# Performance work log

Hardware: AMD Instinct MI355X
Metric: run time of the kernel (lower is better)

Reference implementation:

```python
import jax, jax.numpy as jnp
import numpy as np

B, C, W, H, HEADS = 32, 512, 32, 32, 8
D = C // HEADS
N = W * H
LN_EPS = 1e-5


def setup_inputs() -> dict:
    key = jax.random.key(0)
    ks = jax.random.split(key, 11)
    s = 1.0 / np.sqrt(C)
    return {
        "x": jax.random.normal(ks[0], (B, C, W, H), jnp.float32),
        "Wq": jax.random.normal(ks[1], (C, C), jnp.float32) * s,
        "bq": jax.random.normal(ks[2], (C,), jnp.float32) * 0.01,
        "Wk": jax.random.normal(ks[3], (C, C), jnp.float32) * s,
        "bk": jax.random.normal(ks[4], (C,), jnp.float32) * 0.01,
        "Wv": jax.random.normal(ks[5], (C, C), jnp.float32) * s,
        "bv": jax.random.normal(ks[6], (C,), jnp.float32) * 0.01,
        "rel_h": jax.random.normal(ks[7], (1, HEADS, D, 1, H), jnp.float32),
        "rel_w": jax.random.normal(ks[8], (1, HEADS, D, W, 1), jnp.float32),
        "ln_w": jnp.ones((C, W, H), jnp.float32),
        "ln_b": jnp.zeros((C, W, H), jnp.float32),
    }


def reference(x, Wq, bq, Wk, bk, Wv, bv, rel_h, rel_w, ln_w, ln_b):
    b, c, w, h = x.shape
    nh, d, n = HEADS, c // HEADS, w * h

    def proj(Wm, bm):
        # 1x1 conv == per-pixel linear: out[b,o,w,h] = sum_c Wm[o,c] x[b,c,w,h] + bm[o]
        y = jnp.einsum('bcwh,oc->bowh', x, Wm) + bm[None, :, None, None]
        return y.reshape(b, nh, d, n)

    q = proj(Wq, bq)  # [B,h,d,N]
    k = proj(Wk, bk)
    v = proj(Wv, bv)

    # content-content: q^T k -> [B,h,N,N]
    cc = jnp.einsum('bhdn,bhdm->bhnm', q, k)
    # content-position: (rel_h + rel_w) flattened to [h,d,N], permuted, matmul with q
    pos = (rel_h + rel_w).reshape(nh, d, n)  # [h,d,N]
    cp = jnp.einsum('hdn,bhdm->bhnm', pos, q)

    attn = jax.nn.softmax(cc + cp, axis=-1)  # [B,h,N,N]
    # out = v @ attn^T  -> [B,h,d,N]
    out = jnp.einsum('bhdn,bhmn->bhdm', v, attn)
    out = out.reshape(b, c, w, h)

    # LayerNorm over [C,W,H] with elementwise affine, then residual
    mu = jnp.mean(out, axis=(1, 2, 3), keepdims=True)
    var = jnp.var(out, axis=(1, 2, 3), keepdims=True)
    out = (out - mu) * jax.lax.rsqrt(var + LN_EPS) * ln_w[None] + ln_b[None]
    return out + x
```

## Files before the change

kernel.cpp:

```cpp
#include <hip/hip_runtime.h>
#include <stdint.h>

typedef _Float16 f16x8 __attribute__((ext_vector_type(8)));
typedef _Float16 f16x4 __attribute__((ext_vector_type(4)));
typedef __fp16   fp16x2 __attribute__((ext_vector_type(2)));
typedef float f32x4  __attribute__((ext_vector_type(4)));

__device__ __forceinline__ _Float16 f2h(float f){ return (_Float16)f; }

__device__ __forceinline__ void gl16(const void* g, void* l){
  __builtin_amdgcn_global_load_lds((const __attribute__((address_space(1))) void*)g,
                                   (__attribute__((address_space(3))) void*)l, 16, 0, 0);
}

#define NB   32
#define NC   512
#define NH   8
#define ND   64
#define NN   1024

#define LOG2E 1.44269504f

__global__ __launch_bounds__(256) void wt_conv(const float* __restrict__ Wq,
                                               const float* __restrict__ Wk,
                                               const float* __restrict__ Wv,
                                               _Float16* __restrict__ Wt){
  int idx = blockIdx.x * 256 + threadIdx.x;
  int sel = idx >> 18;
  const float* W = (sel == 0) ? Wq : (sel == 1) ? Wk : Wv;
  Wt[idx] = f2h(W[idx & 262143]);
}

__global__ __launch_bounds__(256) void transpose_x(const float* __restrict__ x,
                                                   _Float16* __restrict__ xT){
  __shared__ float tile[32][33];
  int n0 = blockIdx.x * 32, c0 = blockIdx.y * 32, b = blockIdx.z;
  int t = threadIdx.x;
  int tn = t & 31, tc = t >> 5;
#pragma unroll
  for (int k = 0; k < 4; k++)
    tile[tc + 8*k][tn] = x[(b*NC + c0 + tc + 8*k)*NN + n0 + tn];
  __syncthreads();
#pragma unroll
  for (int k = 0; k < 4; k++)
    xT[(b*NN + n0 + tc + 8*k)*NC + c0 + tn] = f2h(tile[tn][tc + 8*k]);
}

__global__ __launch_bounds__(256) void pos_conv(const float* __restrict__ rel_h,
                                                const float* __restrict__ rel_w,
                                                _Float16* __restrict__ pos_t){
  int idx = blockIdx.x * 256 + threadIdx.x;
  int d = idx & 63, n = (idx >> 6) & 1023, h = idx >> 16;
  int ww = n >> 5, hh = n & 31;
  float v = rel_h[(h*ND + d)*32 + hh] + rel_w[(h*ND + d)*32 + ww];
  pos_t[idx] = f2h(v);
}

#define TSTR 136

__global__ __launch_bounds__(256) void proj_gemm(const _Float16* __restrict__ Wt,
                                                 const _Float16* __restrict__ xT,
                                                 const float* __restrict__ bq,
                                                 const float* __restrict__ bk,
                                                 const float* __restrict__ bv,
                                                 _Float16* __restrict__ q_ws,
                                                 _Float16* __restrict__ k_ws,
                                                 _Float16* __restrict__ v_ws){
  __shared__ _Float16 smem[17408];
  _Float16* As = smem;
  _Float16* Bs = smem + 8192;

  int mt = blockIdx.x;
  int nt = blockIdx.y;
  int b  = blockIdx.z;
  int t = threadIdx.x, lane = t & 63, w = t >> 6;
  int wm = w >> 1, wn = w & 1;
  int lr = lane & 15, lg = lane >> 4;

  f32x4 acc[4][4];
#pragma unroll
  for (int i = 0; i < 4; i++)
#pragma unroll
    for (int j = 0; j < 4; j++) acc[i][j] = (f32x4)0.f;

  const _Float16* Arow = Wt + mt * 128 * NC;
  const _Float16* Brow = xT + (b * NN + nt * 128) * NC;

  int s_r8 = lane >> 3;
  int s_g  = lane & 7;

  for (int k0 = 0; k0 < NC; k0 += 64){
    __syncthreads();
#pragma unroll
    for (int i = 0; i < 4; i++){
      int r0  = w*32 + i*8;
      int row = r0 + s_r8;
      int gx  = (s_g ^ (row & 7)) << 3;
      gl16(Arow + row*NC + k0 + gx, As + r0*64);
      gl16(Brow + row*NC + k0 + gx, Bs + r0*64);
    }
    __syncthreads();
#pragma unroll
    for (int ks = 0; ks < 2; ks++){
      int xg = (((ks << 2) | lg) ^ (lr & 7)) << 3;
      f16x8 af[4], bfr[4];
#pragma unroll
      for (int mi = 0; mi < 4; mi++)
        af[mi] = *(f16x8*)(As + (wm*64 + mi*16 + lr)*64 + xg);
#pragma unroll
      for (int nj = 0; nj < 4; nj++)
        bfr[nj] = *(f16x8*)(Bs + (wn*64 + nj*16 + lr)*64 + xg);
      __builtin_amdgcn_s_setprio(1);
#pragma unroll
      for (int mi = 0; mi < 4; mi++)
#pragma unroll
        for (int nj = 0; nj < 4; nj++)
          acc[mi][nj] = __builtin_amdgcn_mfma_f32_16x16x32_f16(af[mi], bfr[nj], acc[mi][nj], 0, 0, 0);
      __builtin_amdgcn_s_setprio(0);
    }
  }
  __syncthreads();

  if (mt < 8){
    _Float16* Ts = smem;
#pragma unroll
    for (int mi = 0; mi < 4; mi++){
      int o0 = wm*64 + mi*16 + 4*lg;
      int og = mt*128 + o0;
      int sel = og >> 9, oo = og & 511;
      const float* bias = (sel == 0) ? bq : bk;
      float sc = (sel == 0) ? LOG2E : 1.f;
      float b0 = bias[oo], b1 = bias[oo+1], b2 = bias[oo+2], b3 = bias[oo+3];
#pragma unroll
      for (int nj = 0; nj < 4; nj++){
        int pix = wn*64 + nj*16 + lr;
        f16x4 pk;
        pk[0] = f2h((acc[mi][nj][0] + b0) * sc);
        pk[1] = f2h((acc[mi][nj][1] + b1) * sc);
        pk[2] = f2h((acc[mi][nj][2] + b2) * sc);
        pk[3] = f2h((acc[mi][nj][3] + b3) * sc);
        *(f16x4*)(Ts + pix*TSTR + o0) = pk;
      }
    }
    __syncthreads();
#pragma unroll
    for (int i = 0; i < 8; i++){
      int lin = t + 256 * i;
      int c_o = lin & 15, pix = lin >> 4;
      f16x8 v = *(f16x8*)(Ts + pix*TSTR + c_o*8);
      int og = mt*128 + c_o*8;
      int sel = og >> 9, oo = og & 511;
      int head = oo >> 6, d = oo & 63;
      _Float16* dst = (sel == 0) ? q_ws : k_ws;
      *(f16x8*)(dst + (((b*NH + head)*NN) + nt*128 + pix)*ND + d) = v;
    }
  } else {
    _Float16* Ts2 = smem;
#pragma unroll
    for (int mi = 0; mi < 4; mi++){
      int o0 = wm*64 + mi*16 + 4*lg;
      int vb = (mt - 8)*128 + o0;
      float b0 = bv[vb], b1 = bv[vb+1], b2 = bv[vb+2], b3 = bv[vb+3];
#pragma unroll
      for (int nj = 0; nj < 4; nj++){
        int pix = wn*64 + nj*16 + lr;
        Ts2[(o0+0)*TSTR + pix] = f2h(acc[mi][nj][0] + b0);
        Ts2[(o0+1)*TSTR + pix] = f2h(acc[mi][nj][1] + b1);
        Ts2[(o0+2)*TSTR + pix] = f2h(acc[mi][nj][2] + b2);
        Ts2[(o0+3)*TSTR + pix] = f2h(acc[mi][nj][3] + b3);
      }
    }
    __syncthreads();
#pragma unroll
    for (int i = 0; i < 8; i++){
      int lin = t + 256 * i;
      int pix8 = lin & 15, o_loc = lin >> 4;
      f16x8 v = *(f16x8*)(Ts2 + o_loc*TSTR + pix8*8);
      int vb = (mt - 8)*128 + o_loc;
      int head = vb >> 6, d = vb & 63;
      *(f16x8*)(v_ws + ((b*NH + head)*ND + d)*NN + nt*128 + pix8*8) = v;
    }
  }
}

#define KSTR 136
#define PSTR 72
#define OSTR 65
#define OFF_VT 8704
#define OFF_P  12800

__global__ __launch_bounds__(256, 3) void attn_kernel(const _Float16* __restrict__ q_ws,
                                                      const _Float16* __restrict__ k_ws,
                                                      const _Float16* __restrict__ v_ws,
                                                      const _Float16* __restrict__ pos_t,
                                                      _Float16* __restrict__ o16,
                                                      float* __restrict__ red){
  __shared__ _Float16 smem[22016];
  __shared__ float lnred[8];
  _Float16* Kc = smem;
  _Float16* Vt = smem + OFF_VT;
  _Float16* Pl = smem + OFF_P;

  int bid = blockIdx.x;
  int sid = (bid & 7) * 256 + (bid >> 3);
  int qt = sid & 7, h = (sid >> 3) & 7, b = sid >> 6;

  int t = threadIdx.x, lane = t & 63, w = t >> 6;
  int lr = lane & 15, lg = lane >> 4;

  const _Float16* qbh = q_ws + (b*NH + h) * NN * ND;
  const _Float16* kbh = k_ws + (b*NH + h) * NN * ND;
  const _Float16* vbh = v_ws + (b*NH + h) * ND * NN;
  const _Float16* pph = pos_t + h * NN * ND;

  f16x8 qreg[2][4];
#pragma unroll
  for (int qi = 0; qi < 2; qi++){
    int row = qt*128 + w*32 + qi*16 + lr;
#pragma unroll
    for (int ks = 0; ks < 4; ks++){
      const _Float16* src = (ks < 2) ? (qbh + row*ND + ks*32 + lg*8)
                                     : (pph + row*ND + (ks-2)*32 + lg*8);
      qreg[qi][ks] = *(const f16x8*)src;
    }
  }

  f16x8 ones;
#pragma unroll
  for (int e = 0; e < 8; e++) ones[e] = (_Float16)1.f;

  float m_r[2];
  f32x4 oacc[2][4];
  f32x4 lacc[2];
#pragma unroll
  for (int qi = 0; qi < 2; qi++){ m_r[qi] = -1e30f; lacc[qi] = (f32x4)0.f; }
#pragma unroll
  for (int qi = 0; qi < 2; qi++)
#pragma unroll
    for (int dj = 0; dj < 4; dj++) oacc[qi][dj] = (f32x4)0.f;

  for (int n0 = 0; n0 < NN; n0 += 64){
    __syncthreads();
#pragma unroll
    for (int i = 0; i < 4; i++){
      int lin = t + 256*i;
      int row = lin >> 4, c8 = lin & 15;
      const _Float16* src = (c8 < 8) ? (kbh + (n0 + row)*ND + c8*8)
                                     : (qbh + (n0 + row)*ND + (c8 - 8)*8);
      *(f16x8*)(Kc + row*KSTR + c8*8) = *(const f16x8*)src;
    }
#pragma unroll
    for (int i = 0; i < 2; i++){
      int lin = t + 256*i;
      int d = lin >> 3, ch = lin & 7;
      *(f16x8*)(Vt + d*64 + ((ch*8) ^ ((d & 7) << 3))) = *(const f16x8*)(vbh + d*NN + n0 + ch*8);
    }
    __syncthreads();

    f32x4 sacc[4][2];
#pragma unroll
    for (int kt = 0; kt < 4; kt++)
#pragma unroll
      for (int qi = 0; qi < 2; qi++) sacc[kt][qi] = (f32x4)0.f;
    __builtin_amdgcn_s_setprio(1);
#pragma unroll
    for (int ks = 0; ks < 4; ks++){
      f16x8 kf[4];
#pragma unroll
      for (int kt = 0; kt < 4; kt++)
        kf[kt] = *(f16x8*)(Kc + (kt*16 + lr)*KSTR + ks*32 + lg*8);
#pragma unroll
      for (int kt = 0; kt < 4; kt++)
#pragma unroll
        for (int qi = 0; qi < 2; qi++)
          sacc[kt][qi] = __builtin_amdgcn_mfma_f32_16x16x32_f16(kf[kt], qreg[qi][ks], sacc[kt][qi], 0, 0, 0);
    }
    __builtin_amdgcn_s_setprio(0);

#pragma unroll
    for (int qi = 0; qi < 2; qi++){
      float m0 = fmaxf(fmaxf(sacc[0][qi][0], sacc[0][qi][1]), fmaxf(sacc[0][qi][2], sacc[0][qi][3]));
      float m1 = fmaxf(fmaxf(sacc[1][qi][0], sacc[1][qi][1]), fmaxf(sacc[1][qi][2], sacc[1][qi][3]));
      float m2 = fmaxf(fmaxf(sacc[2][qi][0], sacc[2][qi][1]), fmaxf(sacc[2][qi][2], sacc[2][qi][3]));
      float m3 = fmaxf(fmaxf(sacc[3][qi][0], sacc[3][qi][1]), fmaxf(sacc[3][qi][2], sacc[3][qi][3]));
      float mx = fmaxf(fmaxf(m0, m1), fmaxf(m2, m3));
      mx = fmaxf(mx, __shfl_xor(mx, 16));
      mx = fmaxf(mx, __shfl_xor(mx, 32));
      if (!__all(mx - m_r[qi] <= 11.f)){
        float mn2 = fmaxf(m_r[qi], mx);
        float cr = __builtin_exp2f(m_r[qi] - mn2);
        m_r[qi] = mn2;
#pragma unroll
        for (int r = 0; r < 4; r++){
          float crow = __shfl(cr, 4*lg + r);
          lacc[qi][r] *= crow;
#pragma unroll
          for (int dj = 0; dj < 4; dj++) oacc[qi][dj][r] *= crow;
        }
      }
      float mn = m_r[qi];
#pragma unroll
      for (int kt = 0; kt < 4; kt++){
        float p0 = __builtin_exp2f(sacc[kt][qi][0] - mn);
        float p1 = __builtin_exp2f(sacc[kt][qi][1] - mn);
        float p2 = __builtin_exp2f(sacc[kt][qi][2] - mn);
        float p3 = __builtin_exp2f(sacc[kt][qi][3] - mn);
        union { fp16x2 h2[2]; uint2 u2; } pu;
        pu.h2[0] = __builtin_amdgcn_cvt_pkrtz(p0, p1);
        pu.h2[1] = __builtin_amdgcn_cvt_pkrtz(p2, p3);
        *(uint2*)(Pl + (w*32 + qi*16 + lr)*PSTR + kt*16 + lg*4) = pu.u2;
      }
    }

    __builtin_amdgcn_s_setprio(1);
#pragma unroll
    for (int ks = 0; ks < 2; ks++){
      f16x8 pf[2], vf[4];
#pragma unroll
      for (int qi = 0; qi < 2; qi++)
        pf[qi] = *(f16x8*)(Pl + (w*32 + qi*16 + lr)*PSTR + ks*32 + lg*8);
#pragma unroll
      for (int dj = 0; dj < 4; dj++){
        int row = dj*16 + lr;
        vf[dj] = *(f16x8*)(Vt + row*64 + ((ks*32 + lg*8) ^ ((row & 7) << 3)));
      }
#pragma unroll
      for (int qi = 0; qi < 2; qi++){
        lacc[qi] = __builtin_amdgcn_mfma_f32_16x16x32_f16(pf[qi], ones, lacc[qi], 0, 0, 0);
#pragma unroll
        for (int dj = 0; dj < 4; dj++)
          oacc[qi][dj] = __builtin_amdgcn_mfma_f32_16x16x32_f16(pf[qi], vf[dj], oacc[qi][dj], 0, 0, 0);
      }
    }
    __builtin_amdgcn_s_setprio(0);
  }

  float s_ln = 0.f, q_ln = 0.f;
  __syncthreads();
  float* Ot = (float*)smem;
#pragma unroll
  for (int qi = 0; qi < 2; qi++){
#pragma unroll
    for (int r = 0; r < 4; r++){
      float invr = 1.f / lacc[qi][r];
#pragma unroll
      for (int dj = 0; dj < 4; dj++){
        float val = oacc[qi][dj][r] * invr;
        s_ln += val; q_ln += val*val;
        Ot[(w*32 + qi*16 + 4*lg + r)*OSTR + dj*16 + lr] = val;
      }
    }
  }
  __syncthreads();

#pragma unroll
  for (int i = 0; i < 4; i++){
    int lin = t + 256*i;
    int d = lin >> 4, jc = lin & 15;
    f16x8 v;
#pragma unroll
    for (int e = 0; e < 8; e++) v[e] = f2h(Ot[(jc*8 + e)*OSTR + d]);
    *(f16x8*)(o16 + (b*NC + h*ND + d)*NN + qt*128 + jc*8) = v;
  }

#pragma unroll
  for (int off = 1; off < 64; off <<= 1){
    s_ln += __shfl_xor(s_ln, off);
    q_ln += __shfl_xor(q_ln, off);
  }
  if (lane == 0){ lnred[w*2] = s_ln; lnred[w*2 + 1] = q_ln; }
  __syncthreads();
  if (t == 0){
    int idx = ((b*NH + h)*8 + qt)*2;
    red[idx]     = lnred[0] + lnred[2] + lnred[4] + lnred[6];
    red[idx + 1] = lnred[1] + lnred[3] + lnred[5] + lnred[7];
  }
}

__global__ void ln_stats(const float* __restrict__ red, float* __restrict__ stats){
  int b = threadIdx.x;
  if (b < 32){
    float s = 0.f, sq = 0.f;
    for (int j = 0; j < 64; j++){ s += red[(b*64 + j)*2]; sq += red[(b*64 + j)*2 + 1]; }
    float mu  = s * (1.f / 524288.f);
    float var = sq * (1.f / 524288.f) - mu*mu;
    stats[b*2] = mu;
    stats[b*2 + 1] = rsqrtf(var + 1e-5f);
  }
}

__global__ __launch_bounds__(256) void ln_apply(const float* __restrict__ x,
                                                const _Float16* __restrict__ o16,
                                                const float* __restrict__ lw,
                                                const float* __restrict__ lb,
                                                const float* __restrict__ stats,
                                                float* __restrict__ out){
  int tid = blockIdx.x*256 + threadIdx.x;
  for (int i8 = tid; i8 < 2097152; i8 += 524288){
    int b = i8 >> 16;
    int r8 = i8 & 65535;
    float mu = stats[b*2], rs = stats[b*2 + 1];
    f16x8 o = *(const f16x8*)(o16 + (size_t)i8*8);
    float4 x0 = ((const float4*)x)[i8*2],  x1 = ((const float4*)x)[i8*2 + 1];
    float4 w0 = ((const float4*)lw)[r8*2], w1 = ((const float4*)lw)[r8*2 + 1];
    float4 b0 = ((const float4*)lb)[r8*2], b1 = ((const float4*)lb)[r8*2 + 1];
    float4 r0, r1;
    r0.x = ((float)o[0] - mu)*rs*w0.x + b0.x + x0.x;
    r0.y = ((float)o[1] - mu)*rs*w0.y + b0.y + x0.y;
    r0.z = ((float)o[2] - mu)*rs*w0.z + b0.z + x0.z;
    r0.w = ((float)o[3] - mu)*rs*w0.w + b0.w + x0.w;
    r1.x = ((float)o[4] - mu)*rs*w1.x + b1.x + x1.x;
    r1.y = ((float)o[5] - mu)*rs*w1.y + b1.y + x1.y;
    r1.z = ((float)o[6] - mu)*rs*w1.z + b1.z + x1.z;
    r1.w = ((float)o[7] - mu)*rs*w1.w + b1.w + x1.w;
    ((float4*)out)[i8*2]     = r0;
    ((float4*)out)[i8*2 + 1] = r1;
  }
}

extern "C" void kernel_launch(void* const* d_in, const int* in_sizes, int n_in,
                              void* d_out, int out_size, void* d_ws, size_t ws_size,
                              hipStream_t stream){
  (void)in_sizes; (void)n_in; (void)out_size; (void)ws_size;
  const float* x    = (const float*)d_in[0];
  const float* Wq   = (const float*)d_in[1];
  const float* bq   = (const float*)d_in[2];
  const float* Wk   = (const float*)d_in[3];
  const float* bk   = (const float*)d_in[4];
  const float* Wv   = (const float*)d_in[5];
  const float* bv   = (const float*)d_in[6];
  const float* relh = (const float*)d_in[7];
  const float* relw = (const float*)d_in[8];
  const float* lnw  = (const float*)d_in[9];
  const float* lnb  = (const float*)d_in[10];
  float* out = (float*)d_out;
  char* ws = (char*)d_ws;

  _Float16* q_ws  = (_Float16*)(ws);
  _Float16* k_ws  = (_Float16*)(ws + 33554432);
  _Float16* v_ws  = (_Float16*)(ws + 67108864);
  _Float16* xT    = (_Float16*)(ws + 100663296);
  _Float16* Wt    = (_Float16*)(ws + 134217728);
  _Float16* pos_t = (_Float16*)(ws + 135790592);
  float* red   = (float*)(ws + 136839168);
  float* stats = red + 4096;
  _Float16* o16 = xT;

  wt_conv    <<<3072, 256, 0, stream>>>(Wq, Wk, Wv, Wt);
  transpose_x<<<dim3(32, 16, 32), 256, 0, stream>>>(x, xT);
  pos_conv   <<<2048, 256, 0, stream>>>(relh, relw, pos_t);
  proj_gemm  <<<dim3(12, 8, 32), 256, 0, stream>>>(Wt, xT, bq, bk, bv, q_ws, k_ws, v_ws);
  attn_kernel<<<2048, 256, 0, stream>>>(q_ws, k_ws, v_ws, pos_t, o16, red);
  ln_stats   <<<1, 64, 0, stream>>>(red, stats);
  ln_apply   <<<2048, 256, 0, stream>>>(x, o16, lnw, lnb, stats, out);
}
```

Baseline: 291.4 us.

## Switch attention MFMAs to 32x32x16 and keep P in registers

Rewrites the attention inner loop to use 32x32x16 MFMA tiles with a transposed output layout, so each lane owns one query column. Softmax probabilities now stay in registers and feed the PV MFMA directly, removing the LDS round-trip for P and the per-row shuffles for the rescale factor. The LDS footprint shrinks and the occupancy hint in launch bounds is dropped. The 16-wide fragment gathers from K and V tiles now use split 4-element loads, which may add LDS bank conflicts.

New measurement: 331.8 us. +13.9%, slower.

```diff
diff --git a/kernel.cpp b/kernel.cpp
--- a/kernel.cpp
+++ b/kernel.cpp
@@ -5,6 +5,7 @@
 typedef _Float16 f16x4 __attribute__((ext_vector_type(4)));
 typedef __fp16   fp16x2 __attribute__((ext_vector_type(2)));
 typedef float f32x4  __attribute__((ext_vector_type(4)));
+typedef float f32x16 __attribute__((ext_vector_type(16)));
 
 __device__ __forceinline__ _Float16 f2h(float f){ return (_Float16)f; }
 
@@ -184,44 +185,46 @@
 }
 
 #define KSTR 136
-#define PSTR 72
 #define OSTR 65
 #define OFF_VT 8704
-#define OFF_P  12800
-
-__global__ __launch_bounds__(256, 3) void attn_kernel(const _Float16* __restrict__ q_ws,
-                                                      const _Float16* __restrict__ k_ws,
-                                                      const _Float16* __restrict__ v_ws,
-                                                      const _Float16* __restrict__ pos_t,
-                                                      _Float16* __restrict__ o16,
-                                                      float* __restrict__ red){
-  __shared__ _Float16 smem[22016];
+
+__global__ __launch_bounds__(256) void attn_kernel(const _Float16* __restrict__ q_ws,
+                                                   const _Float16* __restrict__ k_ws,
+                                                   const _Float16* __restrict__ v_ws,
+                                                   const _Float16* __restrict__ pos_t,
+                                                   _Float16* __restrict__ o16,
+                                                   float* __restrict__ red){
+  __shared__ _Float16 smem[16640];
   __shared__ float lnred[8];
   _Float16* Kc = smem;
   _Float16* Vt = smem + OFF_VT;
-  _Float16* Pl = smem + OFF_P;
 
   int bid = blockIdx.x;
   int sid = (bid & 7) * 256 + (bid >> 3);
   int qt = sid & 7, h = (sid >> 3) & 7, b = sid >> 6;
 
   int t = threadIdx.x, lane = t & 63, w = t >> 6;
-  int lr = lane & 15, lg = lane >> 4;
+  int qc = lane & 31, hf = lane >> 5;
+  int h4 = hf << 2;
 
   const _Float16* qbh = q_ws + (b*NH + h) * NN * ND;
   const _Float16* kbh = k_ws + (b*NH + h) * NN * ND;
   const _Float16* vbh = v_ws + (b*NH + h) * ND * NN;
   const _Float16* pph = pos_t + h * NN * ND;
 
-  f16x8 qreg[2][4];
-#pragma unroll
-  for (int qi = 0; qi < 2; qi++){
-    int row = qt*128 + w*32 + qi*16 + lr;
-#pragma unroll
-    for (int ks = 0; ks < 4; ks++){
-      const _Float16* src = (ks < 2) ? (qbh + row*ND + ks*32 + lg*8)
-                                     : (pph + row*ND + (ks-2)*32 + lg*8);
-      qreg[qi][ks] = *(const f16x8*)src;
+  union v8u { f16x4 v4[2]; f16x8 v8; };
+
+  f16x8 qreg[8];
+  {
+    int row = qt*128 + w*32 + qc;
+#pragma unroll
+    for (int ks = 0; ks < 8; ks++){
+      int c = (ks & 3) * 16;
+      const _Float16* src = (ks < 4) ? (qbh + row*ND + c) : (pph + row*ND + c);
+      v8u u;
+      u.v4[0] = *(const f16x4*)(src + h4);
+      u.v4[1] = *(const f16x4*)(src + 8 + h4);
+      qreg[ks] = u.v8;
     }
   }
 
@@ -229,15 +232,10 @@
 #pragma unroll
   for (int e = 0; e < 8; e++) ones[e] = (_Float16)1.f;
 
-  float m_r[2];
-  f32x4 oacc[2][4];
-  f32x4 lacc[2];
-#pragma unroll
-  for (int qi = 0; qi < 2; qi++){ m_r[qi] = -1e30f; lacc[qi] = (f32x4)0.f; }
-#pragma unroll
-  for (int qi = 0; qi < 2; qi++)
-#pragma unroll
-    for (int dj = 0; dj < 4; dj++) oacc[qi][dj] = (f32x4)0.f;
+  float m_r = -1e30f;
+  f32x16 oacc[2];
+  f32x16 lacc = (f32x16)0.f;
+  oacc[0] = (f32x16)0.f; oacc[1] = (f32x16)0.f;
 
   for (int n0 = 0; n0 < NN; n0 += 64){
     __syncthreads();
@@ -257,80 +255,70 @@
     }
     __syncthreads();
 
-    f32x4 sacc[4][2];
-#pragma unroll
-    for (int kt = 0; kt < 4; kt++)
-#pragma unroll
-      for (int qi = 0; qi < 2; qi++) sacc[kt][qi] = (f32x4)0.f;
+    f32x16 sacc[2];
+    sacc[0] = (f32x16)0.f; sacc[1] = (f32x16)0.f;
     __builtin_amdgcn_s_setprio(1);
 #pragma unroll
-    for (int ks = 0; ks < 4; ks++){
-      f16x8 kf[4];
-#pragma unroll
-      for (int kt = 0; kt < 4; kt++)
-        kf[kt] = *(f16x8*)(Kc + (kt*16 + lr)*KSTR + ks*32 + lg*8);
-#pragma unroll
-      for (int kt = 0; kt < 4; kt++)
-#pragma unroll
-        for (int qi = 0; qi < 2; qi++)
-          sacc[kt][qi] = __builtin_amdgcn_mfma_f32_16x16x32_f16(kf[kt], qreg[qi][ks], sacc[kt][qi], 0, 0, 0);
+    for (int ks = 0; ks < 8; ks++){
+      int cb = ks*16 + h4;
+#pragma unroll
+      for (int kt = 0; kt < 2; kt++){
+        const _Float16* kr = Kc + (kt*32 + qc)*KSTR + cb;
+        v8u u;
+        u.v4[0] = *(const f16x4*)(kr);
+        u.v4[1] = *(const f16x4*)(kr + 8);
+        sacc[kt] = __builtin_amdgcn_mfma_f32_32x32x16_f16(u.v8, qreg[ks], sacc[kt], 0, 0, 0);
+      }
     }
     __builtin_amdgcn_s_setprio(0);
 
-#pragma unroll
-    for (int qi = 0; qi < 2; qi++){
-      float m0 = fmaxf(fmaxf(sacc[0][qi][0], sacc[0][qi][1]), fmaxf(sacc[0][qi][2], sacc[0][qi][3]));
-      float m1 = fmaxf(fmaxf(sacc[1][qi][0], sacc[1][qi][1]), fmaxf(sacc[1][qi][2], sacc[1][qi][3]));
-      float m2 = fmaxf(fmaxf(sacc[2][qi][0], sacc[2][qi][1]), fmaxf(sacc[2][qi][2], sacc[2][qi][3]));
-      float m3 = fmaxf(fmaxf(sacc[3][qi][0], sacc[3][qi][1]), fmaxf(sacc[3][qi][2], sacc[3][qi][3]));
-      float mx = fmaxf(fmaxf(m0, m1), fmaxf(m2, m3));
-      mx = fmaxf(mx, __shfl_xor(mx, 16));
+    {
+      float mx = sacc[0][0];
+#pragma unroll
+      for (int r = 1; r < 16; r++) mx = fmaxf(mx, sacc[0][r]);
+#pragma unroll
+      for (int r = 0; r < 16; r++) mx = fmaxf(mx, sacc[1][r]);
       mx = fmaxf(mx, __shfl_xor(mx, 32));
-      if (!__all(mx - m_r[qi] <= 11.f)){
-        float mn2 = fmaxf(m_r[qi], mx);
-        float cr = __builtin_exp2f(m_r[qi] - mn2);
-        m_r[qi] = mn2;
-#pragma unroll
-        for (int r = 0; r < 4; r++){
-          float crow = __shfl(cr, 4*lg + r);
-          lacc[qi][r] *= crow;
-#pragma unroll
-          for (int dj = 0; dj < 4; dj++) oacc[qi][dj][r] *= crow;
-        }
-      }
-      float mn = m_r[qi];
-#pragma unroll
-      for (int kt = 0; kt < 4; kt++){
-        float p0 = __builtin_exp2f(sacc[kt][qi][0] - mn);
-        float p1 = __builtin_exp2f(sacc[kt][qi][1] - mn);
-        float p2 = __builtin_exp2f(sacc[kt][qi][2] - mn);
-        float p3 = __builtin_exp2f(sacc[kt][qi][3] - mn);
-        union { fp16x2 h2[2]; uint2 u2; } pu;
-        pu.h2[0] = __builtin_amdgcn_cvt_pkrtz(p0, p1);
-        pu.h2[1] = __builtin_amdgcn_cvt_pkrtz(p2, p3);
-        *(uint2*)(Pl + (w*32 + qi*16 + lr)*PSTR + kt*16 + lg*4) = pu.u2;
-      }
-    }
+      if (!__all(mx - m_r <= 11.f)){
+        float mn2 = fmaxf(m_r, mx);
+        float cr = __builtin_exp2f(m_r - mn2);
+        m_r = mn2;
+        lacc *= cr;
+        oacc[0] *= cr; oacc[1] *= cr;
+      }
+    }
+    float mn = m_r;
 
     __builtin_amdgcn_s_setprio(1);
 #pragma unroll
-    for (int ks = 0; ks < 2; ks++){
-      f16x8 pf[2], vf[4];
-#pragma unroll
-      for (int qi = 0; qi < 2; qi++)
-        pf[qi] = *(f16x8*)(Pl + (w*32 + qi*16 + lr)*PSTR + ks*32 + lg*8);
-#pragma unroll
-      for (int dj = 0; dj < 4; dj++){
-        int row = dj*16 + lr;
-        vf[dj] = *(f16x8*)(Vt + row*64 + ((ks*32 + lg*8) ^ ((row & 7) << 3)));
-      }
-#pragma unroll
-      for (int qi = 0; qi < 2; qi++){
-        lacc[qi] = __builtin_amdgcn_mfma_f32_16x16x32_f16(pf[qi], ones, lacc[qi], 0, 0, 0);
-#pragma unroll
-        for (int dj = 0; dj < 4; dj++)
-          oacc[qi][dj] = __builtin_amdgcn_mfma_f32_16x16x32_f16(pf[qi], vf[dj], oacc[qi][dj], 0, 0, 0);
-      }
+    for (int s = 0; s < 4; s++){
+      int kt = s >> 1, rb = (s & 1) << 3;
+      float p0 = __builtin_exp2f(sacc[kt][rb+0] - mn);
+      float p1 = __builtin_exp2f(sacc[kt][rb+1] - mn);
+      float p2 = __builtin_exp2f(sacc[kt][rb+2] - mn);
+      float p3 = __builtin_exp2f(sacc[kt][rb+3] - mn);
+      float p4 = __builtin_exp2f(sacc[kt][rb+4] - mn);
+      float p5 = __builtin_exp2f(sacc[kt][rb+5] - mn);
+      float p6 = __builtin_exp2f(sacc[kt][rb+6] - mn);
+      float p7 = __builtin_exp2f(sacc[kt][rb+7] - mn);
+      union { fp16x2 h2[4]; f16x8 v8; } pe;
+      pe.h2[0] = __builtin_amdgcn_cvt_pkrtz(p0, p1);
+      pe.h2[1] = __builtin_amdgcn_cvt_pkrtz(p2, p3);
+      pe.h2[2] = __builtin_amdgcn_cvt_pkrtz(p4, p5);
+      pe.h2[3] = __builtin_amdgcn_cvt_pkrtz(p6, p7);
+      f16x8 vf[2];
+#pragma unroll
+      for (int dt = 0; dt < 2; dt++){
+        int row = dt*32 + qc;
+        int sw = (row & 7) << 3;
+        v8u u;
+        u.v4[0] = *(const f16x4*)(Vt + row*64 + ((16*s) ^ sw) + h4);
+        u.v4[1] = *(const f16x4*)(Vt + row*64 + ((16*s + 8) ^ sw) + h4);
+        vf[dt] = u.v8;
+      }
+      lacc = __builtin_amdgcn_mfma_f32_32x32x16_f16(ones, pe.v8, lacc, 0, 0, 0);
+      oacc[0] = __builtin_amdgcn_mfma_f32_32x32x16_f16(vf[0], pe.v8, oacc[0], 0, 0, 0);
+      oacc[1] = __builtin_amdgcn_mfma_f32_32x32x16_f16(vf[1], pe.v8, oacc[1], 0, 0, 0);
     }
     __builtin_amdgcn_s_setprio(0);
   }
@@ -338,16 +326,17 @@
   float s_ln = 0.f, q_ln = 0.f;
   __syncthreads();
   float* Ot = (float*)smem;
-#pragma unroll
-  for (int qi = 0; qi < 2; qi++){
-#pragma unroll
-    for (int r = 0; r < 4; r++){
-      float invr = 1.f / lacc[qi][r];
-#pragma unroll
-      for (int dj = 0; dj < 4; dj++){
-        float val = oacc[qi][dj][r] * invr;
+  {
+    float inv = 1.f / lacc[0];
+    int qrow = w*32 + qc;
+#pragma unroll
+    for (int dt = 0; dt < 2; dt++){
+#pragma unroll
+      for (int r = 0; r < 16; r++){
+        int d = dt*32 + (r & 3) + ((r >> 2) << 3) + h4;
+        float val = oacc[dt][r] * inv;
         s_ln += val; q_ln += val*val;
-        Ot[(w*32 + qi*16 + 4*lg + r)*OSTR + dj*16 + lr] = val;
+        Ot[qrow*OSTR + d] = val;
       }
     }
   }
```
